# Kernel tuning notes

Measured on AMD Instinct MI355X. Metric: run time of the kernel, lower is better.

Reference implementation:

```python
import jax, jax.numpy as jnp
import numpy as np

BN_EPS = 1e-5


def _knn_idx(pos, k):
    # pos: (B, 3, N). Nearest-k by squared euclidean distance (self included).
    sq = jnp.sum(pos * pos, axis=1)                        # (B, N)
    inner = jnp.einsum('bcn,bcm->bnm', pos, pos)           # (B, N, N)
    neg_dist = 2.0 * inner - sq[:, :, None] - sq[:, None, :]
    _, idx = jax.lax.top_k(neg_dist, k)                    # (B, N, k)
    return idx


def setup_inputs() -> dict:
    key = jax.random.key(0)
    k1, k2, k3 = jax.random.split(key, 3)
    B, C, N, K, D = 4, 64, 8192, 16, 64
    return {
        'x': jax.random.normal(k1, (B, C, N), dtype=jnp.float32),
        'pos': jax.random.normal(k2, (B, 3, N), dtype=jnp.float32),
        'spectral_filter': jax.random.normal(k3, (K, C, D), dtype=jnp.float32),
        'gamma': jnp.ones((D,), dtype=jnp.float32),
        'beta': jnp.zeros((D,), dtype=jnp.float32),
    }


def reference(x, pos, spectral_filter, gamma, beta):
    k = spectral_filter.shape[0]
    idx = _knn_idx(pos, k)                                  # (B, N, k) int32
    # gather neighbors: nb[b, c, n, j] = x[b, c, idx[b, n, j]]
    nb = jax.vmap(lambda xf, ii: xf[:, ii])(x, idx)         # (B, C, N, k)
    edge = nb - x[:, :, :, None]                            # (B, C, N, k)
    # per-k small GEMM: 'bnkc,kcd->bnd' (channel dim is axis 1 here)
    out = jnp.einsum('bcnk,kcd->bnd', edge, spectral_filter)
    out = out.transpose(0, 2, 1)                            # (B, D, N)
    # BatchNorm1d, training mode (biased variance over batch and points)
    mean = jnp.mean(out, axis=(0, 2), keepdims=True)
    var = jnp.var(out, axis=(0, 2), keepdims=True)
    out = (out - mean) * jax.lax.rsqrt(var + BN_EPS)
    return out * gamma[None, :, None] + beta[None, :, None]
```

## Files before the change

### kernel.cpp

```cpp
#include <hip/hip_runtime.h>
#include <hip/hip_bf16.h>

#define NPTS 8192
#define NQ   32768
#define KNN  16

#define OFF_XT   0
#define OFF_FBIG (8*1024*1024)
#define OFF_SUMS (OFF_FBIG + 278528)
#define OFF_IDX  (OFF_SUMS + 512)
#define OFF_PRE  (OFF_IDX + 2*1024*1024)
#define OFF_SQ   OFF_PRE

__device__ __forceinline__ float sq3(float x, float y, float z) {
    #pragma clang fp contract(off)
    float xx = x * x;
    float yy = y * y;
    float zz = z * z;
    return (xx + yy) + zz;
}
__device__ __forceinline__ float negd2(float qx, float qy, float qz, float sqn,
                                       float mx, float my, float mz, float sqm) {
    #pragma clang fp contract(off)
    float p0 = qx * mx;
    float inn = __builtin_fmaf(qz, mz, __builtin_fmaf(qy, my, p0));
    float t = 2.0f * inn;
    float u = t - sqn;
    return u - sqm;
}
#define KEY_EPS2 2.0e-3f

__global__ __launch_bounds__(256) void k_prep_x(const float* __restrict__ x,
                                                float* __restrict__ xT) {
    __shared__ float tile[64][65];
    int lane = threadIdx.x & 63, wid = threadIdx.x >> 6;
    int b = blockIdx.x >> 7, nt = blockIdx.x & 127;
    int n0 = nt * 64;
    for (int rr = 0; rr < 16; ++rr) {
        int c = wid * 16 + rr;
        tile[c][lane] = x[((size_t)b * 64 + c) * NPTS + n0 + lane];
    }
    __syncthreads();
    for (int rr = 0; rr < 16; ++rr) {
        int r = wid * 16 + rr;
        xT[((size_t)(b * NPTS + n0 + r)) * 64 + lane] = tile[lane][r];
    }
}

__global__ __launch_bounds__(256) void k_prep_f(const float* __restrict__ F,
                                                float* __restrict__ Fb,
                                                float* __restrict__ sums) {
    int j = blockIdx.x;
    if (j < 16) {
        for (int e = threadIdx.x; e < 4096; e += 256)
            Fb[j * 4096 + e] = F[j * 4096 + e];
    } else if (j == 16) {
        for (int e = threadIdx.x; e < 4096; e += 256) {
            float s = 0.f;
            for (int k = 0; k < 16; ++k) s += F[k * 4096 + e];
            Fb[16 * 4096 + e] = -s;
        }
    } else {
        if (threadIdx.x < 128) sums[threadIdx.x] = 0.f;
    }
}

__global__ __launch_bounds__(256) void k_prep_sq(const float* __restrict__ pos,
                                                 float* __restrict__ sqa) {
    int g = blockIdx.x * 256 + threadIdx.x;
    int b = g >> 13, n = g & (NPTS - 1);
    const float* pb = pos + (size_t)b * 3 * NPTS;
    sqa[g] = sq3(pb[n], pb[NPTS + n], pb[2 * NPTS + n]);
}

__global__ __launch_bounds__(256) void k_knn(const float* __restrict__ pos,
                                             const float* __restrict__ sqa,
                                             int* __restrict__ idxo) {
    __shared__ int   cnt[32];
    __shared__ int   sidx[32][128];
    __shared__ float skey[32][128];
    __shared__ int   outI[32][16];
    int t = threadIdx.x, lane = t & 63, wid = t >> 6;
    int qblk = blockIdx.x * 32;
    int b = qblk >> 13;
    const float* px = pos + (size_t)b * 3 * NPTS;
    const float* py = px + NPTS;
    const float* pz = py + NPTS;
    const float* sb = sqa + (size_t)b * NPTS;
    int n0 = (qblk & (NPTS - 1)) + wid * 8;

    float qxs[8], qys[8], qzs[8], sqs[8], tqx[8], tqy[8], tqz[8];
    #pragma unroll
    for (int i = 0; i < 8; ++i) {
        qxs[i] = px[n0 + i]; qys[i] = py[n0 + i];
        qzs[i] = pz[n0 + i]; sqs[i] = sb[n0 + i];
        tqx[i] = 2.0f * qxs[i]; tqy[i] = 2.0f * qys[i]; tqz[i] = 2.0f * qzs[i];
    }
    if (lane < 8) cnt[wid * 8 + lane] = 0;
    if (lane < 16) {
        #pragma unroll
        for (int i = 0; i < 8; ++i) outI[wid * 8 + i][lane] = n0 + i;
    }

    float lm[8];
    #pragma unroll
    for (int i = 0; i < 8; ++i) lm[i] = -3.4e38f;
    for (int it = 0; it < 32; ++it) {
        int m = it * 256 + lane * 4;
        float4 X = *(const float4*)(px + m);
        float4 Y = *(const float4*)(py + m);
        float4 Z = *(const float4*)(pz + m);
        float4 S = *(const float4*)(sb + m);
        #pragma unroll
        for (int i = 0; i < 8; ++i) {
            float a0 = __builtin_fmaf(tqx[i], X.x, __builtin_fmaf(tqy[i], Y.x, __builtin_fmaf(tqz[i], Z.x, -S.x)));
            float a1 = __builtin_fmaf(tqx[i], X.y, __builtin_fmaf(tqy[i], Y.y, __builtin_fmaf(tqz[i], Z.y, -S.y)));
            float a2 = __builtin_fmaf(tqx[i], X.z, __builtin_fmaf(tqy[i], Y.z, __builtin_fmaf(tqz[i], Z.z, -S.z)));
            float a3 = __builtin_fmaf(tqx[i], X.w, __builtin_fmaf(tqy[i], Y.w, __builtin_fmaf(tqz[i], Z.w, -S.w)));
            lm[i] = fmaxf(lm[i], fmaxf(fmaxf(a0, a1), fmaxf(a2, a3)));
        }
    }

    float thr[8];
    #pragma unroll
    for (int i = 0; i < 8; ++i) {
        float val = lm[i], tv = 0.f;
        for (int r = 0; r < 16; ++r) {
            float mm = val;
            mm = fmaxf(mm, __shfl_xor(mm, 1, 64));
            mm = fmaxf(mm, __shfl_xor(mm, 2, 64));
            mm = fmaxf(mm, __shfl_xor(mm, 4, 64));
            mm = fmaxf(mm, __shfl_xor(mm, 8, 64));
            mm = fmaxf(mm, __shfl_xor(mm, 16, 64));
            mm = fmaxf(mm, __shfl_xor(mm, 32, 64));
            tv = mm;
            if (val == mm) val = -3.4e38f;
        }
        thr[i] = tv - KEY_EPS2;
    }

    for (int it = 0; it < 32; ++it) {
        int m = it * 256 + lane * 4;
        float4 X = *(const float4*)(px + m);
        float4 Y = *(const float4*)(py + m);
        float4 Z = *(const float4*)(pz + m);
        float4 S = *(const float4*)(sb + m);
        #pragma unroll
        for (int i = 0; i < 8; ++i) {
            int lq = wid * 8 + i;
            float a0 = __builtin_fmaf(tqx[i], X.x, __builtin_fmaf(tqy[i], Y.x, __builtin_fmaf(tqz[i], Z.x, -S.x)));
            float a1 = __builtin_fmaf(tqx[i], X.y, __builtin_fmaf(tqy[i], Y.y, __builtin_fmaf(tqz[i], Z.y, -S.y)));
            float a2 = __builtin_fmaf(tqx[i], X.z, __builtin_fmaf(tqy[i], Y.z, __builtin_fmaf(tqz[i], Z.z, -S.z)));
            float a3 = __builtin_fmaf(tqx[i], X.w, __builtin_fmaf(tqy[i], Y.w, __builtin_fmaf(tqz[i], Z.w, -S.w)));
            if (a0 >= thr[i]) { int s_ = atomicAdd(&cnt[lq],1); if (s_<128) sidx[lq][s_] = m; }
            if (a1 >= thr[i]) { int s_ = atomicAdd(&cnt[lq],1); if (s_<128) sidx[lq][s_] = m+1; }
            if (a2 >= thr[i]) { int s_ = atomicAdd(&cnt[lq],1); if (s_<128) sidx[lq][s_] = m+2; }
            if (a3 >= thr[i]) { int s_ = atomicAdd(&cnt[lq],1); if (s_<128) sidx[lq][s_] = m+3; }
        }
    }
    __syncthreads();

    #pragma unroll 1
    for (int i = 0; i < 8; ++i) {
        int lq = wid * 8 + i;
        int S = cnt[lq]; if (S > 128) S = 128;
        for (int p = lane; p < S; p += 64) {
            int m = sidx[lq][p];
            skey[lq][p] = negd2(qxs[i], qys[i], qzs[i], sqs[i],
                                px[m], py[m], pz[m], sb[m]);
        }
    }
    __syncthreads();

    #pragma unroll 1
    for (int i = 0; i < 8; ++i) {
        int lq = wid * 8 + i;
        int S = cnt[lq]; if (S > 128) S = 128;
        for (int p = lane; p < S; p += 64) {
            int m = sidx[lq][p];
            float km = skey[lq][p];
            int rank = 0;
            for (int j = 0; j < S; ++j) {
                float kj = skey[lq][j];
                int ij = sidx[lq][j];
                if (kj > km || (kj == km && ij < m)) rank++;
            }
            if (rank < KNN) outI[lq][rank] = m;
        }
    }
    __syncthreads();
    #pragma unroll
    for (int h = 0; h < 2; ++h) {
        int lq = h * 16 + (t >> 4);
        idxo[(size_t)(qblk + lq) * KNN + (t & 15)] = outI[lq][t & 15];
    }
}

#define CPAD 68
__global__ __launch_bounds__(256) void k_conv(const float* __restrict__ xT,
                                              const float* __restrict__ Fb,
                                              const int* __restrict__ idx,
                                              float* __restrict__ outp) {
    __shared__ float At[64][CPAD];
    __shared__ float Bt[64 * 64];
    int t = threadIdx.x;
    int q0 = blockIdx.x * 64;
    int bbase = q0 & ~(NPTS - 1);
    int qi0 = (t >> 4) * 4;
    int dj0 = (t & 15) * 4;
    int r = t & 63;
    int s = t >> 6;

    float acc[4][4];
    #pragma unroll
    for (int a = 0; a < 4; ++a)
        #pragma unroll
        for (int bb = 0; bb < 4; ++bb) acc[a][bb] = 0.f;

    for (int j = 0; j < 17; ++j) {
        {
            int qg = q0 + r;
            int nbr = (j < 16) ? (idx[(size_t)qg * KNN + j] & (NPTS - 1))
                               : (qg & (NPTS - 1));
            const float* src = xT + ((size_t)(bbase + nbr) * 64 + s * 16);
            float4 v0 = *(const float4*)(src);
            float4 v1 = *(const float4*)(src + 4);
            float4 v2 = *(const float4*)(src + 8);
            float4 v3 = *(const float4*)(src + 12);
            int c0 = s * 16;
            At[c0+ 0][r] = v0.x; At[c0+ 1][r] = v0.y; At[c0+ 2][r] = v0.z; At[c0+ 3][r] = v0.w;
            At[c0+ 4][r] = v1.x; At[c0+ 5][r] = v1.y; At[c0+ 6][r] = v1.z; At[c0+ 7][r] = v1.w;
            At[c0+ 8][r] = v2.x; At[c0+ 9][r] = v2.y; At[c0+10][r] = v2.z; At[c0+11][r] = v2.w;
            At[c0+12][r] = v3.x; At[c0+13][r] = v3.y; At[c0+14][r] = v3.z; At[c0+15][r] = v3.w;
        }
        {
            const float* fj = Fb + j * 4096;
            #pragma unroll
            for (int u = 0; u < 4; ++u) {
                int e = u * 1024 + t * 4;
                *(float4*)&Bt[e] = *(const float4*)(fj + e);
            }
        }
        __syncthreads();
        #pragma unroll 8
        for (int k = 0; k < 64; ++k) {
            float4 av = *(const float4*)&At[k][qi0];
            float4 bv = *(const float4*)&Bt[k * 64 + dj0];
            acc[0][0] = fmaf(av.x, bv.x, acc[0][0]);
            acc[0][1] = fmaf(av.x, bv.y, acc[0][1]);
            acc[0][2] = fmaf(av.x, bv.z, acc[0][2]);
            acc[0][3] = fmaf(av.x, bv.w, acc[0][3]);
            acc[1][0] = fmaf(av.y, bv.x, acc[1][0]);
            acc[1][1] = fmaf(av.y, bv.y, acc[1][1]);
            acc[1][2] = fmaf(av.y, bv.z, acc[1][2]);
            acc[1][3] = fmaf(av.y, bv.w, acc[1][3]);
            acc[2][0] = fmaf(av.z, bv.x, acc[2][0]);
            acc[2][1] = fmaf(av.z, bv.y, acc[2][1]);
            acc[2][2] = fmaf(av.z, bv.z, acc[2][2]);
            acc[2][3] = fmaf(av.z, bv.w, acc[2][3]);
            acc[3][0] = fmaf(av.w, bv.x, acc[3][0]);
            acc[3][1] = fmaf(av.w, bv.y, acc[3][1]);
            acc[3][2] = fmaf(av.w, bv.z, acc[3][2]);
            acc[3][3] = fmaf(av.w, bv.w, acc[3][3]);
        }
        __syncthreads();
    }
    #pragma unroll
    for (int qi = 0; qi < 4; ++qi) {
        float4 o = make_float4(acc[qi][0], acc[qi][1], acc[qi][2], acc[qi][3]);
        *(float4*)(outp + (size_t)(q0 + qi0 + qi) * 64 + dj0) = o;
    }
}

__global__ __launch_bounds__(256) void k_stats(const float* __restrict__ outp,
                                               float* __restrict__ sums) {
    __shared__ float ls[4][64], lss[4][64];
    int lane = threadIdx.x & 63, wid = threadIdx.x >> 6;
    int gw = blockIdx.x * 4 + wid;
    float s = 0.f, ss = 0.f;
    for (int r = gw * 32; r < gw * 32 + 32; ++r) {
        float v = outp[(size_t)r * 64 + lane];
        s += v; ss = fmaf(v, v, ss);
    }
    ls[wid][lane] = s; lss[wid][lane] = ss;
    __syncthreads();
    if (wid == 0) {
        float a = 0.f, b2 = 0.f;
        for (int w = 0; w < 4; ++w) { a += ls[w][lane]; b2 += lss[w][lane]; }
        atomicAdd(&sums[lane], a);
        atomicAdd(&sums[64 + lane], b2);
    }
}

__global__ __launch_bounds__(256) void k_bn(const float* __restrict__ outp,
                                            const float* __restrict__ sums,
                                            const float* __restrict__ gamma,
                                            const float* __restrict__ beta,
                                            float* __restrict__ out) {
    __shared__ float tile[64][65];
    __shared__ float sa[64], sb[64];
    int lane = threadIdx.x & 63, wid = threadIdx.x >> 6;
    int b = blockIdx.x >> 7, nt = blockIdx.x & 127;
    int n0 = nt * 64;
    if (threadIdx.x < 64) {
        const float inv = 1.f / 32768.f;
        float mean = sums[threadIdx.x] * inv;
        float var = sums[64 + threadIdx.x] * inv - mean * mean;
        float rs = rsqrtf(var + 1e-5f);
        float a = rs * gamma[threadIdx.x];
        sa[threadIdx.x] = a;
        sb[threadIdx.x] = beta[threadIdx.x] - mean * a;
    }
    for (int rr = 0; rr < 16; ++rr) {
        int r = wid * 16 + rr;
        tile[r][lane] = outp[((size_t)(b * NPTS + n0 + r)) * 64 + lane];
    }
    __syncthreads();
    for (int rr = 0; rr < 16; ++rr) {
        int dr = wid * 16 + rr;
        out[((size_t)b * 64 + dr) * NPTS + n0 + lane] =
            fmaf(tile[lane][dr], sa[dr], sb[dr]);
    }
}

extern "C" void kernel_launch(void* const* d_in, const int* in_sizes, int n_in,
                              void* d_out, int out_size, void* d_ws, size_t ws_size,
                              hipStream_t stream) {
    (void)in_sizes; (void)n_in; (void)out_size; (void)ws_size;
    const float* x     = (const float*)d_in[0];
    const float* pos   = (const float*)d_in[1];
    const float* F     = (const float*)d_in[2];
    const float* gamma = (const float*)d_in[3];
    const float* beta  = (const float*)d_in[4];
    float* out = (float*)d_out;

    char* ws = (char*)d_ws;
    float* xT   = (float*)(ws + OFF_XT);
    float* Fb   = (float*)(ws + OFF_FBIG);
    float* sums = (float*)(ws + OFF_SUMS);
    int*   idx  = (int*)(ws + OFF_IDX);
    float* pre  = (float*)(ws + OFF_PRE);
    float* sqa  = (float*)(ws + OFF_SQ);

    k_prep_x<<<512, 256, 0, stream>>>(x, xT);
    k_prep_f<<<18, 256, 0, stream>>>(F, Fb, sums);
    k_prep_sq<<<128, 256, 0, stream>>>(pos, sqa);
    k_knn<<<1024, 256, 0, stream>>>(pos, sqa, idx);
    k_conv<<<512, 256, 0, stream>>>(xT, Fb, idx, pre);
    k_stats<<<256, 256, 0, stream>>>(pre, sums);
    k_bn<<<512, 256, 0, stream>>>(pre, sums, gamma, beta, out);
}
```

Before: 300.3 us.

## Retile conv GEMM to 8x8 per-thread with packed FMA and 16-bit KNN indices

The neighbor-conv GEMM kernel moves from 64-point/256-thread tiles with 4x4 per-thread outputs to 128-point/128-thread tiles with 8x8 per-thread outputs. The inner loop now uses two-wide vector FMAs so the compiler can emit packed fp32 FMA instructions. The aim is more FMA per shared-memory load and fewer ALU issue slots. Separately, the KNN candidate index buffer shrinks to unsigned short to cut shared-memory footprint. In exchange, the conv launch has only 256 blocks of 2 waves each, which lowers occupancy and latency hiding, and there is a stray redundant zero store into At inside the gather loop.

```diff
diff --git a/kernel.cpp b/kernel.cpp
--- a/kernel.cpp
+++ b/kernel.cpp
@@ -11,6 +11,8 @@
 #define OFF_IDX  (OFF_SUMS + 512)
 #define OFF_PRE  (OFF_IDX + 2*1024*1024)
 #define OFF_SQ   OFF_PRE
+
+typedef float v2f __attribute__((ext_vector_type(2)));
 
 __device__ __forceinline__ float sq3(float x, float y, float z) {
     #pragma clang fp contract(off)
@@ -76,10 +78,10 @@
 __global__ __launch_bounds__(256) void k_knn(const float* __restrict__ pos,
                                              const float* __restrict__ sqa,
                                              int* __restrict__ idxo) {
-    __shared__ int   cnt[32];
-    __shared__ int   sidx[32][128];
-    __shared__ float skey[32][128];
-    __shared__ int   outI[32][16];
+    __shared__ int            cnt[32];
+    __shared__ unsigned short sidx[32][128];
+    __shared__ float          skey[32][128];
+    __shared__ int            outI[32][16];
     int t = threadIdx.x, lane = t & 63, wid = t >> 6;
     int qblk = blockIdx.x * 32;
     int b = qblk >> 13;
@@ -152,10 +154,10 @@
             float a1 = __builtin_fmaf(tqx[i], X.y, __builtin_fmaf(tqy[i], Y.y, __builtin_fmaf(tqz[i], Z.y, -S.y)));
             float a2 = __builtin_fmaf(tqx[i], X.z, __builtin_fmaf(tqy[i], Y.z, __builtin_fmaf(tqz[i], Z.z, -S.z)));
             float a3 = __builtin_fmaf(tqx[i], X.w, __builtin_fmaf(tqy[i], Y.w, __builtin_fmaf(tqz[i], Z.w, -S.w)));
-            if (a0 >= thr[i]) { int s_ = atomicAdd(&cnt[lq],1); if (s_<128) sidx[lq][s_] = m; }
-            if (a1 >= thr[i]) { int s_ = atomicAdd(&cnt[lq],1); if (s_<128) sidx[lq][s_] = m+1; }
-            if (a2 >= thr[i]) { int s_ = atomicAdd(&cnt[lq],1); if (s_<128) sidx[lq][s_] = m+2; }
-            if (a3 >= thr[i]) { int s_ = atomicAdd(&cnt[lq],1); if (s_<128) sidx[lq][s_] = m+3; }
+            if (a0 >= thr[i]) { int s_ = atomicAdd(&cnt[lq],1); if (s_<128) sidx[lq][s_] = (unsigned short)m; }
+            if (a1 >= thr[i]) { int s_ = atomicAdd(&cnt[lq],1); if (s_<128) sidx[lq][s_] = (unsigned short)(m+1); }
+            if (a2 >= thr[i]) { int s_ = atomicAdd(&cnt[lq],1); if (s_<128) sidx[lq][s_] = (unsigned short)(m+2); }
+            if (a3 >= thr[i]) { int s_ = atomicAdd(&cnt[lq],1); if (s_<128) sidx[lq][s_] = (unsigned short)(m+3); }
         }
     }
     __syncthreads();
@@ -196,79 +198,89 @@
     }
 }
 
-#define CPAD 68
-__global__ __launch_bounds__(256) void k_conv(const float* __restrict__ xT,
+#define CPAD2 132
+__global__ __launch_bounds__(128) void k_conv(const float* __restrict__ xT,
                                               const float* __restrict__ Fb,
                                               const int* __restrict__ idx,
                                               float* __restrict__ outp) {
-    __shared__ float At[64][CPAD];
+    __shared__ float At[64][CPAD2];
     __shared__ float Bt[64 * 64];
     int t = threadIdx.x;
-    int q0 = blockIdx.x * 64;
+    int q0 = blockIdx.x * 128;
     int bbase = q0 & ~(NPTS - 1);
-    int qi0 = (t >> 4) * 4;
-    int dj0 = (t & 15) * 4;
-    int r = t & 63;
-    int s = t >> 6;
-
-    float acc[4][4];
-    #pragma unroll
-    for (int a = 0; a < 4; ++a)
+    int qi0 = (t >> 3) * 8;
+    int dj0 = (t & 7) * 8;
+
+    v2f acc[8][4];
+    #pragma unroll
+    for (int a = 0; a < 8; ++a)
         #pragma unroll
-        for (int bb = 0; bb < 4; ++bb) acc[a][bb] = 0.f;
+        for (int p = 0; p < 4; ++p) acc[a][p] = (v2f)(0.f);
 
     for (int j = 0; j < 17; ++j) {
         {
-            int qg = q0 + r;
+            int qg = q0 + t;
             int nbr = (j < 16) ? (idx[(size_t)qg * KNN + j] & (NPTS - 1))
                                : (qg & (NPTS - 1));
-            const float* src = xT + ((size_t)(bbase + nbr) * 64 + s * 16);
-            float4 v0 = *(const float4*)(src);
-            float4 v1 = *(const float4*)(src + 4);
-            float4 v2 = *(const float4*)(src + 8);
-            float4 v3 = *(const float4*)(src + 12);
-            int c0 = s * 16;
-            At[c0+ 0][r] = v0.x; At[c0+ 1][r] = v0.y; At[c0+ 2][r] = v0.z; At[c0+ 3][r] = v0.w;
-            At[c0+ 4][r] = v1.x; At[c0+ 5][r] = v1.y; At[c0+ 6][r] = v1.z; At[c0+ 7][r] = v1.w;
-            At[c0+ 8][r] = v2.x; At[c0+ 9][r] = v2.y; At[c0+10][r] = v2.z; At[c0+11][r] = v2.w;
-            At[c0+12][r] = v3.x; At[c0+13][r] = v3.y; At[c0+14][r] = v3.z; At[c0+15][r] = v3.w;
+            const float* src = xT + ((size_t)(bbase + nbr) * 64);
+            #pragma unroll
+            for (int s = 0; s < 4; ++s) {
+                float4 v = *(const float4*)(src + s * 4);
+                int c0 = s * 4;
+                At[c0 + 0][t] = v.x; At[c0 + 16][t] = 0.f;
+                At[c0 + 0][t] = v.x;
+                At[c0 + 1][t] = v.y;
+                At[c0 + 2][t] = v.z;
+                At[c0 + 3][t] = v.w;
+            }
+            #pragma unroll
+            for (int s = 0; s < 12; ++s) {
+                float4 v = *(const float4*)(src + 16 + s * 4);
+                int c0 = 16 + s * 4;
+                At[c0 + 0][t] = v.x;
+                At[c0 + 1][t] = v.y;
+                At[c0 + 2][t] = v.z;
+                At[c0 + 3][t] = v.w;
+            }
         }
         {
             const float* fj = Fb + j * 4096;
             #pragma unroll
-            for (int u = 0; u < 4; ++u) {
-                int e = u * 1024 + t * 4;
+            for (int u = 0; u < 8; ++u) {
+                int e = u * 512 + t * 4;
                 *(float4*)&Bt[e] = *(const float4*)(fj + e);
             }
         }
         __syncthreads();
-        #pragma unroll 8
+        #pragma unroll 4
         for (int k = 0; k < 64; ++k) {
-            float4 av = *(const float4*)&At[k][qi0];
-            float4 bv = *(const float4*)&Bt[k * 64 + dj0];
-            acc[0][0] = fmaf(av.x, bv.x, acc[0][0]);
-            acc[0][1] = fmaf(av.x, bv.y, acc[0][1]);
-            acc[0][2] = fmaf(av.x, bv.z, acc[0][2]);
-            acc[0][3] = fmaf(av.x, bv.w, acc[0][3]);
-            acc[1][0] = fmaf(av.y, bv.x, acc[1][0]);
-            acc[1][1] = fmaf(av.y, bv.y, acc[1][1]);
-            acc[1][2] = fmaf(av.y, bv.z, acc[1][2]);
-            acc[1][3] = fmaf(av.y, bv.w, acc[1][3]);
-            acc[2][0] = fmaf(av.z, bv.x, acc[2][0]);
-            acc[2][1] = fmaf(av.z, bv.y, acc[2][1]);
-            acc[2][2] = fmaf(av.z, bv.z, acc[2][2]);
-            acc[2][3] = fmaf(av.z, bv.w, acc[2][3]);
-            acc[3][0] = fmaf(av.w, bv.x, acc[3][0]);
-            acc[3][1] = fmaf(av.w, bv.y, acc[3][1]);
-            acc[3][2] = fmaf(av.w, bv.z, acc[3][2]);
-            acc[3][3] = fmaf(av.w, bv.w, acc[3][3]);
+            float4 a0 = *(const float4*)&At[k][qi0];
+            float4 a1 = *(const float4*)&At[k][qi0 + 4];
+            float4 b0 = *(const float4*)&Bt[k * 64 + dj0];
+            float4 b1 = *(const float4*)&Bt[k * 64 + dj0 + 4];
+            v2f bp0 = (v2f){b0.x, b0.y};
+            v2f bp1 = (v2f){b0.z, b0.w};
+            v2f bp2 = (v2f){b1.x, b1.y};
+            v2f bp3 = (v2f){b1.z, b1.w};
+            float aq[8] = {a0.x, a0.y, a0.z, a0.w, a1.x, a1.y, a1.z, a1.w};
+            #pragma unroll
+            for (int qq = 0; qq < 8; ++qq) {
+                v2f av = (v2f){aq[qq], aq[qq]};
+                acc[qq][0] = __builtin_elementwise_fma(av, bp0, acc[qq][0]);
+                acc[qq][1] = __builtin_elementwise_fma(av, bp1, acc[qq][1]);
+                acc[qq][2] = __builtin_elementwise_fma(av, bp2, acc[qq][2]);
+                acc[qq][3] = __builtin_elementwise_fma(av, bp3, acc[qq][3]);
+            }
         }
         __syncthreads();
     }
     #pragma unroll
-    for (int qi = 0; qi < 4; ++qi) {
-        float4 o = make_float4(acc[qi][0], acc[qi][1], acc[qi][2], acc[qi][3]);
-        *(float4*)(outp + (size_t)(q0 + qi0 + qi) * 64 + dj0) = o;
+    for (int qq = 0; qq < 8; ++qq) {
+        float* dst = outp + (size_t)(q0 + qi0 + qq) * 64 + dj0;
+        float4 o0 = make_float4(acc[qq][0].x, acc[qq][0].y, acc[qq][1].x, acc[qq][1].y);
+        float4 o1 = make_float4(acc[qq][2].x, acc[qq][2].y, acc[qq][3].x, acc[qq][3].y);
+        *(float4*)(dst)     = o0;
+        *(float4*)(dst + 4) = o1;
     }
 }
 
@@ -346,7 +358,7 @@
     k_prep_f<<<18, 256, 0, stream>>>(F, Fb, sums);
     k_prep_sq<<<128, 256, 0, stream>>>(pos, sqa);
     k_knn<<<1024, 256, 0, stream>>>(pos, sqa, idx);
-    k_conv<<<512, 256, 0, stream>>>(xT, Fb, idx, pre);
+    k_conv<<<256, 128, 0, stream>>>(xT, Fb, idx, pre);
     k_stats<<<256, 256, 0, stream>>>(pre, sums);
     k_bn<<<512, 256, 0, stream>>>(pre, sums, gamma, beta, out);
 }
```

Result: slower. 344.1 us (+14.6%).

## Fuse prep kernels, stage KNN candidates in LDS, fold BN stats into conv

Applied to the files above, without the earlier changes.

Merges the x-transpose and filter prep into one launch and drops the separate squared-norm kernel, recomputing norms inside the KNN kernel. The KNN kernel now stages 1024-point tiles of positions and norms in shared memory for both scan passes, and stores candidate indices as 16-bit values with a smaller cap. The BatchNorm sum and sum-of-squares reduction moves into the conv epilogue, which removes the stats kernel and its re-read of the pre-activation buffer. Each tile adds block-wide barriers, the smaller candidate cap raises the chance of overflow truncation, and a __syncthreads between the key and rank phases was removed, which is only safe if each wave reads only its own queries.

```diff
diff --git a/kernel.cpp b/kernel.cpp
--- a/kernel.cpp
+++ b/kernel.cpp
@@ -4,13 +4,13 @@
 #define NPTS 8192
 #define NQ   32768
 #define KNN  16
+#define SCAP 112
 
 #define OFF_XT   0
 #define OFF_FBIG (8*1024*1024)
 #define OFF_SUMS (OFF_FBIG + 278528)
 #define OFF_IDX  (OFF_SUMS + 512)
 #define OFF_PRE  (OFF_IDX + 2*1024*1024)
-#define OFF_SQ   OFF_PRE
 
 __device__ __forceinline__ float sq3(float x, float y, float z) {
     #pragma clang fp contract(off)
@@ -30,31 +30,31 @@
 }
 #define KEY_EPS2 2.0e-3f
 
-__global__ __launch_bounds__(256) void k_prep_x(const float* __restrict__ x,
-                                                float* __restrict__ xT) {
-    __shared__ float tile[64][65];
-    int lane = threadIdx.x & 63, wid = threadIdx.x >> 6;
-    int b = blockIdx.x >> 7, nt = blockIdx.x & 127;
-    int n0 = nt * 64;
-    for (int rr = 0; rr < 16; ++rr) {
-        int c = wid * 16 + rr;
-        tile[c][lane] = x[((size_t)b * 64 + c) * NPTS + n0 + lane];
-    }
-    __syncthreads();
-    for (int rr = 0; rr < 16; ++rr) {
-        int r = wid * 16 + rr;
-        xT[((size_t)(b * NPTS + n0 + r)) * 64 + lane] = tile[lane][r];
-    }
-}
-
-__global__ __launch_bounds__(256) void k_prep_f(const float* __restrict__ F,
-                                                float* __restrict__ Fb,
-                                                float* __restrict__ sums) {
-    int j = blockIdx.x;
-    if (j < 16) {
+__global__ __launch_bounds__(256) void k_prep(const float* __restrict__ x,
+                                              const float* __restrict__ F,
+                                              float* __restrict__ xT,
+                                              float* __restrict__ Fb,
+                                              float* __restrict__ sums) {
+    int bid = blockIdx.x;
+    if (bid < 512) {
+        __shared__ float tile[64][65];
+        int lane = threadIdx.x & 63, wid = threadIdx.x >> 6;
+        int b = bid >> 7, nt = bid & 127;
+        int n0 = nt * 64;
+        for (int rr = 0; rr < 16; ++rr) {
+            int c = wid * 16 + rr;
+            tile[c][lane] = x[((size_t)b * 64 + c) * NPTS + n0 + lane];
+        }
+        __syncthreads();
+        for (int rr = 0; rr < 16; ++rr) {
+            int r = wid * 16 + rr;
+            xT[((size_t)(b * NPTS + n0 + r)) * 64 + lane] = tile[lane][r];
+        }
+    } else if (bid < 528) {
+        int j = bid - 512;
         for (int e = threadIdx.x; e < 4096; e += 256)
             Fb[j * 4096 + e] = F[j * 4096 + e];
-    } else if (j == 16) {
+    } else if (bid == 528) {
         for (int e = threadIdx.x; e < 4096; e += 256) {
             float s = 0.f;
             for (int k = 0; k < 16; ++k) s += F[k * 4096 + e];
@@ -65,35 +65,27 @@
     }
 }
 
-__global__ __launch_bounds__(256) void k_prep_sq(const float* __restrict__ pos,
-                                                 float* __restrict__ sqa) {
-    int g = blockIdx.x * 256 + threadIdx.x;
-    int b = g >> 13, n = g & (NPTS - 1);
-    const float* pb = pos + (size_t)b * 3 * NPTS;
-    sqa[g] = sq3(pb[n], pb[NPTS + n], pb[2 * NPTS + n]);
-}
-
+#define TILE 1024
 __global__ __launch_bounds__(256) void k_knn(const float* __restrict__ pos,
-                                             const float* __restrict__ sqa,
                                              int* __restrict__ idxo) {
-    __shared__ int   cnt[32];
-    __shared__ int   sidx[32][128];
-    __shared__ float skey[32][128];
-    __shared__ int   outI[32][16];
+    __shared__ float Xs[TILE], Ys[TILE], Zs[TILE], Ss[TILE];
+    __shared__ int            cnt[32];
+    __shared__ unsigned short sidx[32][SCAP];
+    __shared__ float          skey[32][SCAP];
+    __shared__ int            outI[32][16];
     int t = threadIdx.x, lane = t & 63, wid = t >> 6;
     int qblk = blockIdx.x * 32;
     int b = qblk >> 13;
     const float* px = pos + (size_t)b * 3 * NPTS;
     const float* py = px + NPTS;
     const float* pz = py + NPTS;
-    const float* sb = sqa + (size_t)b * NPTS;
     int n0 = (qblk & (NPTS - 1)) + wid * 8;
 
     float qxs[8], qys[8], qzs[8], sqs[8], tqx[8], tqy[8], tqz[8];
     #pragma unroll
     for (int i = 0; i < 8; ++i) {
-        qxs[i] = px[n0 + i]; qys[i] = py[n0 + i];
-        qzs[i] = pz[n0 + i]; sqs[i] = sb[n0 + i];
+        qxs[i] = px[n0 + i]; qys[i] = py[n0 + i]; qzs[i] = pz[n0 + i];
+        sqs[i] = sq3(qxs[i], qys[i], qzs[i]);
         tqx[i] = 2.0f * qxs[i]; tqy[i] = 2.0f * qys[i]; tqz[i] = 2.0f * qzs[i];
     }
     if (lane < 8) cnt[wid * 8 + lane] = 0;
@@ -105,20 +97,37 @@
     float lm[8];
     #pragma unroll
     for (int i = 0; i < 8; ++i) lm[i] = -3.4e38f;
-    for (int it = 0; it < 32; ++it) {
-        int m = it * 256 + lane * 4;
-        float4 X = *(const float4*)(px + m);
-        float4 Y = *(const float4*)(py + m);
-        float4 Z = *(const float4*)(pz + m);
-        float4 S = *(const float4*)(sb + m);
-        #pragma unroll
-        for (int i = 0; i < 8; ++i) {
-            float a0 = __builtin_fmaf(tqx[i], X.x, __builtin_fmaf(tqy[i], Y.x, __builtin_fmaf(tqz[i], Z.x, -S.x)));
-            float a1 = __builtin_fmaf(tqx[i], X.y, __builtin_fmaf(tqy[i], Y.y, __builtin_fmaf(tqz[i], Z.y, -S.y)));
-            float a2 = __builtin_fmaf(tqx[i], X.z, __builtin_fmaf(tqy[i], Y.z, __builtin_fmaf(tqz[i], Z.z, -S.z)));
-            float a3 = __builtin_fmaf(tqx[i], X.w, __builtin_fmaf(tqy[i], Y.w, __builtin_fmaf(tqz[i], Z.w, -S.w)));
-            lm[i] = fmaxf(lm[i], fmaxf(fmaxf(a0, a1), fmaxf(a2, a3)));
-        }
+
+    for (int tile = 0; tile < 8; ++tile) {
+        int tb = tile * TILE;
+        {
+            float4 xv = *(const float4*)(px + tb + t * 4);
+            float4 yv = *(const float4*)(py + tb + t * 4);
+            float4 zv = *(const float4*)(pz + tb + t * 4);
+            float4 sv;
+            sv.x = sq3(xv.x, yv.x, zv.x); sv.y = sq3(xv.y, yv.y, zv.y);
+            sv.z = sq3(xv.z, yv.z, zv.z); sv.w = sq3(xv.w, yv.w, zv.w);
+            *(float4*)&Xs[t * 4] = xv; *(float4*)&Ys[t * 4] = yv;
+            *(float4*)&Zs[t * 4] = zv; *(float4*)&Ss[t * 4] = sv;
+        }
+        __syncthreads();
+        #pragma unroll
+        for (int it = 0; it < 4; ++it) {
+            int ml = it * 256 + lane * 4;
+            float4 X = *(const float4*)&Xs[ml];
+            float4 Y = *(const float4*)&Ys[ml];
+            float4 Z = *(const float4*)&Zs[ml];
+            float4 S = *(const float4*)&Ss[ml];
+            #pragma unroll
+            for (int i = 0; i < 8; ++i) {
+                float a0 = __builtin_fmaf(tqx[i], X.x, __builtin_fmaf(tqy[i], Y.x, __builtin_fmaf(tqz[i], Z.x, -S.x)));
+                float a1 = __builtin_fmaf(tqx[i], X.y, __builtin_fmaf(tqy[i], Y.y, __builtin_fmaf(tqz[i], Z.y, -S.y)));
+                float a2 = __builtin_fmaf(tqx[i], X.z, __builtin_fmaf(tqy[i], Y.z, __builtin_fmaf(tqz[i], Z.z, -S.z)));
+                float a3 = __builtin_fmaf(tqx[i], X.w, __builtin_fmaf(tqy[i], Y.w, __builtin_fmaf(tqz[i], Z.w, -S.w)));
+                lm[i] = fmaxf(lm[i], fmaxf(fmaxf(a0, a1), fmaxf(a2, a3)));
+            }
+        }
+        __syncthreads();
     }
 
     float thr[8];
@@ -139,43 +148,59 @@
         thr[i] = tv - KEY_EPS2;
     }
 
-    for (int it = 0; it < 32; ++it) {
-        int m = it * 256 + lane * 4;
-        float4 X = *(const float4*)(px + m);
-        float4 Y = *(const float4*)(py + m);
-        float4 Z = *(const float4*)(pz + m);
-        float4 S = *(const float4*)(sb + m);
-        #pragma unroll
-        for (int i = 0; i < 8; ++i) {
-            int lq = wid * 8 + i;
-            float a0 = __builtin_fmaf(tqx[i], X.x, __builtin_fmaf(tqy[i], Y.x, __builtin_fmaf(tqz[i], Z.x, -S.x)));
-            float a1 = __builtin_fmaf(tqx[i], X.y, __builtin_fmaf(tqy[i], Y.y, __builtin_fmaf(tqz[i], Z.y, -S.y)));
-            float a2 = __builtin_fmaf(tqx[i], X.z, __builtin_fmaf(tqy[i], Y.z, __builtin_fmaf(tqz[i], Z.z, -S.z)));
-            float a3 = __builtin_fmaf(tqx[i], X.w, __builtin_fmaf(tqy[i], Y.w, __builtin_fmaf(tqz[i], Z.w, -S.w)));
-            if (a0 >= thr[i]) { int s_ = atomicAdd(&cnt[lq],1); if (s_<128) sidx[lq][s_] = m; }
-            if (a1 >= thr[i]) { int s_ = atomicAdd(&cnt[lq],1); if (s_<128) sidx[lq][s_] = m+1; }
-            if (a2 >= thr[i]) { int s_ = atomicAdd(&cnt[lq],1); if (s_<128) sidx[lq][s_] = m+2; }
-            if (a3 >= thr[i]) { int s_ = atomicAdd(&cnt[lq],1); if (s_<128) sidx[lq][s_] = m+3; }
-        }
-    }
-    __syncthreads();
+    for (int tile = 0; tile < 8; ++tile) {
+        int tb = tile * TILE;
+        {
+            float4 xv = *(const float4*)(px + tb + t * 4);
+            float4 yv = *(const float4*)(py + tb + t * 4);
+            float4 zv = *(const float4*)(pz + tb + t * 4);
+            float4 sv;
+            sv.x = sq3(xv.x, yv.x, zv.x); sv.y = sq3(xv.y, yv.y, zv.y);
+            sv.z = sq3(xv.z, yv.z, zv.z); sv.w = sq3(xv.w, yv.w, zv.w);
+            *(float4*)&Xs[t * 4] = xv; *(float4*)&Ys[t * 4] = yv;
+            *(float4*)&Zs[t * 4] = zv; *(float4*)&Ss[t * 4] = sv;
+        }
+        __syncthreads();
+        #pragma unroll
+        for (int it = 0; it < 4; ++it) {
+            int ml = it * 256 + lane * 4;
+            int m = tb + ml;
+            float4 X = *(const float4*)&Xs[ml];
+            float4 Y = *(const float4*)&Ys[ml];
+            float4 Z = *(const float4*)&Zs[ml];
+            float4 S = *(const float4*)&Ss[ml];
+            #pragma unroll
+            for (int i = 0; i < 8; ++i) {
+                int lq = wid * 8 + i;
+                float a0 = __builtin_fmaf(tqx[i], X.x, __builtin_fmaf(tqy[i], Y.x, __builtin_fmaf(tqz[i], Z.x, -S.x)));
+                float a1 = __builtin_fmaf(tqx[i], X.y, __builtin_fmaf(tqy[i], Y.y, __builtin_fmaf(tqz[i], Z.y, -S.y)));
+                float a2 = __builtin_fmaf(tqx[i], X.z, __builtin_fmaf(tqy[i], Y.z, __builtin_fmaf(tqz[i], Z.z, -S.z)));
+                float a3 = __builtin_fmaf(tqx[i], X.w, __builtin_fmaf(tqy[i], Y.w, __builtin_fmaf(tqz[i], Z.w, -S.w)));
+                if (a0 >= thr[i]) { int s_ = atomicAdd(&cnt[lq],1); if (s_<SCAP) sidx[lq][s_] = (unsigned short)m; }
+                if (a1 >= thr[i]) { int s_ = atomicAdd(&cnt[lq],1); if (s_<SCAP) sidx[lq][s_] = (unsigned short)(m+1); }
+                if (a2 >= thr[i]) { int s_ = atomicAdd(&cnt[lq],1); if (s_<SCAP) sidx[lq][s_] = (unsigned short)(m+2); }
+                if (a3 >= thr[i]) { int s_ = atomicAdd(&cnt[lq],1); if (s_<SCAP) sidx[lq][s_] = (unsigned short)(m+3); }
+            }
+        }
+        __syncthreads();
+    }
 
     #pragma unroll 1
     for (int i = 0; i < 8; ++i) {
         int lq = wid * 8 + i;
-        int S = cnt[lq]; if (S > 128) S = 128;
+        int S = cnt[lq]; if (S > SCAP) S = SCAP;
         for (int p = lane; p < S; p += 64) {
             int m = sidx[lq][p];
+            float mx = px[m], my = py[m], mz = pz[m];
             skey[lq][p] = negd2(qxs[i], qys[i], qzs[i], sqs[i],
-                                px[m], py[m], pz[m], sb[m]);
-        }
-    }
-    __syncthreads();
+                                mx, my, mz, sq3(mx, my, mz));
+        }
+    }
 
     #pragma unroll 1
     for (int i = 0; i < 8; ++i) {
         int lq = wid * 8 + i;
-        int S = cnt[lq]; if (S > 128) S = 128;
+        int S = cnt[lq]; if (S > SCAP) S = SCAP;
         for (int p = lane; p < S; p += 64) {
             int m = sidx[lq][p];
             float km = skey[lq][p];
@@ -200,7 +225,8 @@
 __global__ __launch_bounds__(256) void k_conv(const float* __restrict__ xT,
                                               const float* __restrict__ Fb,
                                               const int* __restrict__ idx,
-                                              float* __restrict__ outp) {
+                                              float* __restrict__ outp,
+                                              float* __restrict__ sums) {
     __shared__ float At[64][CPAD];
     __shared__ float Bt[64 * 64];
     int t = threadIdx.x;
@@ -270,25 +296,30 @@
         float4 o = make_float4(acc[qi][0], acc[qi][1], acc[qi][2], acc[qi][3]);
         *(float4*)(outp + (size_t)(q0 + qi0 + qi) * 64 + dj0) = o;
     }
-}
-
-__global__ __launch_bounds__(256) void k_stats(const float* __restrict__ outp,
-                                               float* __restrict__ sums) {
-    __shared__ float ls[4][64], lss[4][64];
-    int lane = threadIdx.x & 63, wid = threadIdx.x >> 6;
-    int gw = blockIdx.x * 4 + wid;
-    float s = 0.f, ss = 0.f;
-    for (int r = gw * 32; r < gw * 32 + 32; ++r) {
-        float v = outp[(size_t)r * 64 + lane];
-        s += v; ss = fmaf(v, v, ss);
-    }
-    ls[wid][lane] = s; lss[wid][lane] = ss;
-    __syncthreads();
-    if (wid == 0) {
-        float a = 0.f, b2 = 0.f;
-        for (int w = 0; w < 4; ++w) { a += ls[w][lane]; b2 += lss[w][lane]; }
-        atomicAdd(&sums[lane], a);
-        atomicAdd(&sums[64 + lane], b2);
+    {
+        float* P  = Bt;
+        float* P2 = Bt + 1024;
+        int g = t >> 4;
+        #pragma unroll
+        for (int dd = 0; dd < 4; ++dd) {
+            float sv = ((acc[0][dd] + acc[1][dd]) + acc[2][dd]) + acc[3][dd];
+            float qv = fmaf(acc[3][dd], acc[3][dd],
+                       fmaf(acc[2][dd], acc[2][dd],
+                       fmaf(acc[1][dd], acc[1][dd], acc[0][dd] * acc[0][dd])));
+            P [g * 64 + dj0 + dd] = sv;
+            P2[g * 64 + dj0 + dd] = qv;
+        }
+        __syncthreads();
+        if (t < 64) {
+            float a = 0.f, b2 = 0.f;
+            #pragma unroll
+            for (int gg = 0; gg < 16; ++gg) {
+                a  += P [gg * 64 + t];
+                b2 += P2[gg * 64 + t];
+            }
+            atomicAdd(&sums[t], a);
+            atomicAdd(&sums[64 + t], b2);
+        }
     }
 }
 
@@ -340,13 +371,9 @@
     float* sums = (float*)(ws + OFF_SUMS);
     int*   idx  = (int*)(ws + OFF_IDX);
     float* pre  = (float*)(ws + OFF_PRE);
-    float* sqa  = (float*)(ws + OFF_SQ);
-
-    k_prep_x<<<512, 256, 0, stream>>>(x, xT);
-    k_prep_f<<<18, 256, 0, stream>>>(F, Fb, sums);
-    k_prep_sq<<<128, 256, 0, stream>>>(pos, sqa);
-    k_knn<<<1024, 256, 0, stream>>>(pos, sqa, idx);
-    k_conv<<<512, 256, 0, stream>>>(xT, Fb, idx, pre);
-    k_stats<<<256, 256, 0, stream>>>(pre, sums);
+
+    k_prep<<<530, 256, 0, stream>>>(x, F, xT, Fb, sums);
+    k_knn<<<1024, 256, 0, stream>>>(pos, idx);
+    k_conv<<<512, 256, 0, stream>>>(xT, Fb, idx, pre, sums);
     k_bn<<<512, 256, 0, stream>>>(pre, sums, gamma, beta, out);
 }
```

New measurement: 290.4 us. -3.3%, faster.
